# Kernel tuning notes

Hardware: AMD Instinct MI355X
Metric: run time of the kernel (lower is better)

## Reference

```python
import jax, jax.numpy as jnp
import numpy as np

NUM_HEADS = 12
ROPE_THETA = 10000.0


def setup_inputs() -> dict:
    key = jax.random.key(0)
    ks = jax.random.split(key, 7)
    B, H, W, C = 4, 32, 32, 768
    hd = C // NUM_HEADS
    x = jax.random.normal(ks[0], (B, H, W, C), jnp.float32)
    qkv_w = jax.random.normal(ks[1], (3 * C, C), jnp.float32) * 0.02
    qkv_b = jax.random.normal(ks[2], (3 * C,), jnp.float32) * 0.02
    proj_w = jax.random.normal(ks[3], (C, C), jnp.float32) * 0.02
    proj_b = jax.random.normal(ks[4], (C,), jnp.float32) * 0.02
    rel_pos_h = jax.random.normal(ks[5], (2 * H - 1, hd), jnp.float32) * 0.02
    rel_pos_w = jax.random.normal(ks[6], (2 * W - 1, hd), jnp.float32) * 0.02
    return {"x": x, "qkv_w": qkv_w, "qkv_b": qkv_b, "proj_w": proj_w,
            "proj_b": proj_b, "rel_pos_h": rel_pos_h, "rel_pos_w": rel_pos_w}


def _axial_cis(hd, H, W, theta):
    # compute_axial_cis: frequencies over head_dim//4 bands per axis
    freqs = 1.0 / (theta ** (jnp.arange(0, hd, 4, dtype=jnp.float32)[: hd // 4] / hd))
    t = jnp.arange(H * W, dtype=jnp.float32)
    t_x = t % H          # end_x = input_size[0]
    t_y = jnp.floor(t / H)
    ang = jnp.concatenate([jnp.outer(t_x, freqs), jnp.outer(t_y, freqs)], axis=-1)  # (L, hd//2)
    return jax.lax.complex(jnp.cos(ang), jnp.sin(ang))


def _rope(x, cis):
    # x: (B, nh, L, hd); pairs of channels -> complex, rotate, back to real
    B, nh, L, hd = x.shape
    xr = x.reshape(B, nh, L, hd // 2, 2)
    xc = jax.lax.complex(xr[..., 0], xr[..., 1]) * cis[None, None]
    return jnp.stack([jnp.real(xc), jnp.imag(xc)], axis=-1).reshape(B, nh, L, hd)


def reference(x, qkv_w, qkv_b, proj_w, proj_b, rel_pos_h, rel_pos_w):
    B, H, W, C = x.shape
    nh = NUM_HEADS
    hd = C // nh
    L = H * W
    # fused QKV projection
    qkv = x.reshape(B, L, C) @ qkv_w.T + qkv_b              # (B, L, 3C)
    qkv = qkv.reshape(B, L, 3, nh, hd).transpose(2, 0, 3, 1, 4)
    q, k, v = qkv[0], qkv[1], qkv[2]                        # (B, nh, L, hd)
    # 2D axial RoPE on q, k
    cis = _axial_cis(hd, H, W, ROPE_THETA)
    q = _rope(q, cis)
    k = _rope(k, cis)
    # decomposed relative position bias (math of concat_rel_pos + SDPA w/ rescale)
    coords = jnp.arange(H)[:, None] - jnp.arange(W)[None, :] + (H - 1)  # (H, W), H == W
    Rh = rel_pos_h[coords]                                  # (q_h, k_h, hd)
    Rw = rel_pos_w[coords]                                  # (q_w, k_w, hd)
    rq = q.reshape(B, nh, H, W, hd)
    rel_h = jnp.einsum('bnhwc,hkc->bnhwk', rq, Rh)          # (B, nh, H, W, k_h)
    rel_w = jnp.einsum('bnhwc,wkc->bnhwk', rq, Rw)          # (B, nh, H, W, k_w)
    bias = (rel_h[..., :, None] + rel_w[..., None, :]).reshape(B, nh, L, L)
    scale = 1.0 / jnp.sqrt(jnp.float32(hd))
    scores = jnp.einsum('bnqc,bnkc->bnqk', q, k) * scale + bias
    attn = jax.nn.softmax(scores, axis=-1)
    out = jnp.einsum('bnqk,bnkc->bnqc', attn, v)            # (B, nh, L, hd)
    out = out.transpose(0, 2, 1, 3).reshape(B, H, W, C)
    return out @ proj_w.T + proj_b
```

## Files before the change

kernel.cpp:

```cpp
#include <hip/hip_runtime.h>
#include <hip/hip_bf16.h>
#include <stdint.h>

typedef __hip_bfloat16 bf16;
typedef __attribute__((ext_vector_type(8))) short bf16x8;
typedef __attribute__((ext_vector_type(4))) float f32x4;

#define MFMA16(a, b, c) __builtin_amdgcn_mfma_f32_16x16x32_bf16(a, b, c, 0, 0, 0)

__device__ __forceinline__ void gl_lds16(const void* g, void* l) {
  __builtin_amdgcn_global_load_lds(
      (const __attribute__((address_space(1))) uint32_t*)g,
      (__attribute__((address_space(3))) uint32_t*)l, 16, 0, 0);
}

struct alignas(8) bf16x4s { bf16 a, b, c, d; };

__device__ __forceinline__ void cast4(const float* __restrict__ src,
                                      bf16* __restrict__ dst, int i) {
  float4 v = ((const float4*)src)[i];
  bf16x4s o{__float2bfloat16(v.x), __float2bfloat16(v.y),
            __float2bfloat16(v.z), __float2bfloat16(v.w)};
  ((bf16x4s*)dst)[i] = o;
}

__global__ void k_prep(const float* __restrict__ x, const float* __restrict__ qkvw,
                       const float* __restrict__ projw, bf16* __restrict__ xb,
                       bf16* __restrict__ wqkvb, bf16* __restrict__ wprojb,
                       float* __restrict__ cosT, float* __restrict__ sinT) {
  const int bid = blockIdx.x, tid = threadIdx.x;
  if (bid < 3072) {
    cast4(x, xb, bid * 256 + tid);
  } else if (bid < 4800) {
    cast4(qkvw, wqkvb, (bid - 3072) * 256 + tid);
  } else if (bid < 5376) {
    cast4(projw, wprojb, (bid - 4800) * 256 + tid);
  } else {
    const int i = (bid - 5376) * 256 + tid;
    const int pos = i >> 5, p = i & 31;
    const int j = p & 15;
    const float t = (p < 16) ? (float)(pos & 31) : (float)(pos >> 5);
    const float f = powf(10000.0f, -(float)j / 16.0f);
    float sv, cv;
    sincosf(t * f, &sv, &cv);
    cosT[i] = cv;
    sinT[i] = sv;
  }
}

template <int BM, int BN>
__device__ __forceinline__ void gemm_loop(const bf16* __restrict__ A,
                                          const bf16* __restrict__ Bt,
                                          int m0, int n0, bf16* ldsA, bf16* ldsB,
                                          f32x4* acc) {
  constexpr int FM = BM / 32, FN = BN / 32;
  constexpr int AL = BM / 64, BL = BN / 64;
  constexpr int ABYTES = BM * 64, BBYTES = BN * 64;
  const int tid = threadIdx.x;
  const int lane = tid & 63, w = tid >> 6;
  const int wm = w >> 1, wn = w & 1;
  const int lr = lane & 15, lg = lane >> 4;

  auto stage = [&](int kt, int buf) {
#pragma unroll
    for (int c = 0; c < AL; ++c) {
      const int o = c * 4096 + w * 1024 + lane * 16;
      gl_lds16((const char*)A + ((size_t)(m0 + (o >> 6)) * 768 + kt) * 2 + (o & 63),
               (char*)ldsA + buf * ABYTES + c * 4096 + w * 1024);
    }
#pragma unroll
    for (int c = 0; c < BL; ++c) {
      const int o = c * 4096 + w * 1024 + lane * 16;
      gl_lds16((const char*)Bt + ((size_t)(n0 + (o >> 6)) * 768 + kt) * 2 + (o & 63),
               (char*)ldsB + buf * BBYTES + c * 4096 + w * 1024);
    }
  };

  stage(0, 0);
  int cur = 0;
  for (int ki = 0; ki < 24; ++ki) {
    if (ki + 1 < 24) {
      stage((ki + 1) * 32, cur ^ 1);
      if constexpr (AL + BL == 2) asm volatile("s_waitcnt vmcnt(2)" ::: "memory");
      else if constexpr (AL + BL == 3) asm volatile("s_waitcnt vmcnt(3)" ::: "memory");
      else asm volatile("s_waitcnt vmcnt(4)" ::: "memory");
    } else {
      asm volatile("s_waitcnt vmcnt(0)" ::: "memory");
    }
    __builtin_amdgcn_s_barrier();
    const char* baseA = (const char*)ldsA + cur * ABYTES;
    const char* baseB = (const char*)ldsB + cur * BBYTES;
    bf16x8 af[FM], bf_[FN];
#pragma unroll
    for (int f = 0; f < FM; ++f)
      af[f] = *(const bf16x8*)(baseA + (wm * (BM / 2) + f * 16 + lr) * 64 + lg * 16);
#pragma unroll
    for (int f = 0; f < FN; ++f)
      bf_[f] = *(const bf16x8*)(baseB + (wn * (BN / 2) + f * 16 + lr) * 64 + lg * 16);
    __builtin_amdgcn_s_setprio(1);
#pragma unroll
    for (int fm = 0; fm < FM; ++fm)
#pragma unroll
      for (int fn = 0; fn < FN; ++fn)
        acc[fm * FN + fn] = MFMA16(bf_[fn], af[fm], acc[fm * FN + fn]);
    __builtin_amdgcn_s_setprio(0);
    asm volatile("s_waitcnt lgkmcnt(0)" ::: "memory");
    __builtin_amdgcn_s_barrier();
    cur ^= 1;
  }
}

__global__ __launch_bounds__(256, 6) void k_qkv(
    const bf16* __restrict__ xb, const bf16* __restrict__ wb, const float* __restrict__ qkvb,
    const float* __restrict__ cosT, const float* __restrict__ sinT,
    bf16* __restrict__ Qb, bf16* __restrict__ Kb, bf16* __restrict__ VbT) {
  __shared__ __align__(16) bf16 ldsA[2][64 * 32];
  __shared__ __align__(16) bf16 ldsB[2][128 * 32];
  const int m0 = (blockIdx.x & 63) * 64, n0 = (blockIdx.x >> 6) * 128;
  f32x4 acc[2 * 4] = {};
  gemm_loop<64, 128>(xb, wb, m0, n0, &ldsA[0][0], &ldsB[0][0], acc);
  const int lane = threadIdx.x & 63, w = threadIdx.x >> 6;
  const int wm = w >> 1, wn = w & 1, lr = lane & 15, lg = lane >> 4;
#pragma unroll
  for (int fm = 0; fm < 2; ++fm) {
    const int m = m0 + wm * 32 + fm * 16 + lr;
    const int bb = m >> 10, pos = m & 1023;
#pragma unroll
    for (int fn = 0; fn < 4; ++fn) {
      const int nb = n0 + wn * 64 + fn * 16 + lg * 4;
      const int sect = nb / 768;
      const int cnb = nb - sect * 768;
      const int head = cnb >> 6, db = cnb & 63;
      const float4 b4 = *(const float4*)(qkvb + nb);
      const f32x4 a = acc[fm * 4 + fn];
      const float v0 = a[0] + b4.x, v1 = a[1] + b4.y;
      const float v2 = a[2] + b4.z, v3 = a[3] + b4.w;
      const size_t base = (size_t)(bb * 12 + head) * 65536;
      if (sect < 2) {
        const int p0 = db >> 1;
        const float c0 = cosT[pos * 32 + p0], s0 = sinT[pos * 32 + p0];
        const float c1 = cosT[pos * 32 + p0 + 1], s1 = sinT[pos * 32 + p0 + 1];
        short4 st;
        ((bf16*)&st)[0] = __float2bfloat16(v0 * c0 - v1 * s0);
        ((bf16*)&st)[1] = __float2bfloat16(v1 * c0 + v0 * s0);
        ((bf16*)&st)[2] = __float2bfloat16(v2 * c1 - v3 * s1);
        ((bf16*)&st)[3] = __float2bfloat16(v3 * c1 + v2 * s1);
        bf16* dst = (sect == 0 ? Qb : Kb) + base + (size_t)pos * 64 + db;
        *(short4*)dst = st;
      } else {
        VbT[base + (size_t)(db + 0) * 1024 + pos] = __float2bfloat16(v0);
        VbT[base + (size_t)(db + 1) * 1024 + pos] = __float2bfloat16(v1);
        VbT[base + (size_t)(db + 2) * 1024 + pos] = __float2bfloat16(v2);
        VbT[base + (size_t)(db + 3) * 1024 + pos] = __float2bfloat16(v3);
      }
    }
  }
}

__global__ __launch_bounds__(256) void k_relbias(
    const bf16* __restrict__ Qb, const float* __restrict__ relph,
    const float* __restrict__ relpw, float* __restrict__ relh,
    float* __restrict__ relw) {
  const int bid = blockIdx.x;
  const int bn = bid >> 4;
  const int rem = bid & 15;
  const bool isW = (rem >> 3) != 0;
  const int w = threadIdx.x >> 6;
  const int rc = (rem & 7) * 4 + w;
  const int lane = threadIdx.x & 63;
  const int lr = lane & 15, lg = lane >> 4;
  const float* __restrict__ relp = isW ? relpw : relph;

  bf16x8 af[2][2];
#pragma unroll
  for (int mb = 0; mb < 2; ++mb) {
    const int m = mb * 16 + lr;
    const int l = isW ? (m * 32 + rc) : (rc * 32 + m);
    const bf16* ap = Qb + (size_t)bn * 65536 + (size_t)l * 64 + lg * 8;
#pragma unroll
    for (int ks = 0; ks < 2; ++ks) af[mb][ks] = *(const bf16x8*)(ap + ks * 32);
  }
  bf16x8 bfr[2][2];
#pragma unroll
  for (int nb = 0; nb < 2; ++nb) {
    const int n = nb * 16 + lr;
    const float* bp = relp + (size_t)(31 + rc - n) * 64 + lg * 8;
#pragma unroll
    for (int ks = 0; ks < 2; ++ks) {
      const float4 f0 = *(const float4*)(bp + ks * 32);
      const float4 f1 = *(const float4*)(bp + ks * 32 + 4);
      bf16x8 t;
      ((bf16*)&t)[0] = __float2bfloat16(f0.x);
      ((bf16*)&t)[1] = __float2bfloat16(f0.y);
      ((bf16*)&t)[2] = __float2bfloat16(f0.z);
      ((bf16*)&t)[3] = __float2bfloat16(f0.w);
      ((bf16*)&t)[4] = __float2bfloat16(f1.x);
      ((bf16*)&t)[5] = __float2bfloat16(f1.y);
      ((bf16*)&t)[6] = __float2bfloat16(f1.z);
      ((bf16*)&t)[7] = __float2bfloat16(f1.w);
      bfr[nb][ks] = t;
    }
  }
  f32x4 acc[2][2] = {};
#pragma unroll
  for (int ks = 0; ks < 2; ++ks)
#pragma unroll
    for (int mb = 0; mb < 2; ++mb)
#pragma unroll
      for (int nb = 0; nb < 2; ++nb)
        acc[mb][nb] = MFMA16(af[mb][ks], bfr[nb][ks], acc[mb][nb]);
  float* __restrict__ dst = isW ? relw : relh;
#pragma unroll
  for (int mb = 0; mb < 2; ++mb)
#pragma unroll
    for (int nb = 0; nb < 2; ++nb)
#pragma unroll
      for (int r = 0; r < 4; ++r) {
        const int mo = mb * 16 + lg * 4 + r;
        const int n = nb * 16 + lr;
        const int l = isW ? (mo * 32 + rc) : (rc * 32 + mo);
        dst[(size_t)bn * 32768 + (size_t)l * 32 + n] = acc[mb][nb][r];
      }
}

__global__ __launch_bounds__(256, 3) void k_attn(
    const bf16* __restrict__ Qb, const bf16* __restrict__ Kb, const bf16* __restrict__ VbT,
    const float* __restrict__ relh, const float* __restrict__ relw, bf16* __restrict__ attno) {
  __shared__ __align__(16) bf16 Kt[2][64 * 64];
  __shared__ __align__(16) bf16 Vt[2][64 * 64];
  __shared__ __align__(16) float bH[64 * 33];
  __shared__ __align__(16) bf16 Pl[4][16 * 64];
  const int blk0 = blockIdx.x;
  const int blk = (blk0 & 7) * 96 + (blk0 >> 3);
  const int bn = blk >> 4, qt = blk & 15;
  const int b = bn / 12, head = bn - b * 12;
  const int tid = threadIdx.x;
  const int lane = tid & 63, w = tid >> 6;
  const int lr = lane & 15, lg = lane >> 4;
  const size_t qkvbase = (size_t)bn * 65536;

  auto stageKV = [&](int kt, int buf) {
#pragma unroll
    for (int c = 0; c < 2; ++c) {
      const int off = c * 4096 + w * 1024 + lane * 16;
      const int row = off >> 7;
      const int loff = off ^ ((row & 7) << 4);
      gl_lds16((const char*)Kb + (qkvbase + (size_t)kt * 4096) * 2 + loff,
               (char*)Kt + buf * 8192 + c * 4096 + w * 1024);
      gl_lds16((const char*)VbT + (qkvbase + (size_t)row * 1024 + (size_t)kt * 64) * 2 + (loff & 127),
               (char*)Vt + buf * 8192 + c * 4096 + w * 1024);
    }
  };

  stageKV(0, 0);
  {
    const int r = tid >> 2, q8 = (tid & 3) * 8;
    const float* src = relh + (size_t)bn * 32768 + (size_t)(qt * 64 + r) * 32 + q8;
#pragma unroll
    for (int jj = 0; jj < 8; ++jj) bH[r * 33 + q8 + jj] = src[jj];
  }
  const int qrow_g = qt * 64 + w * 16 + lr;
  float bw[2][4];
  {
    const float* rw = relw + (size_t)bn * 32768 + (size_t)qrow_g * 32;
#pragma unroll
    for (int s1 = 0; s1 < 2; ++s1)
#pragma unroll
      for (int r = 0; r < 4; ++r) bw[s1][r] = rw[s1 * 16 + lg * 4 + r];
  }
  bf16x8 qf[2];
  {
    const char* qp = (const char*)(Qb + qkvbase + (size_t)qrow_g * 64);
    qf[0] = *(const bf16x8*)(qp + lg * 16);
    qf[1] = *(const bf16x8*)(qp + 64 + lg * 16);
  }
  f32x4 oacc[4] = {};
  float psum = 0.0f;
  int cur = 0;

  for (int kt = 0; kt < 16; ++kt) {
    if (kt + 1 < 16) {
      stageKV(kt + 1, cur ^ 1);
      asm volatile("s_waitcnt vmcnt(4)" ::: "memory");
    } else {
      asm volatile("s_waitcnt vmcnt(0)" ::: "memory");
    }
    __builtin_amdgcn_s_barrier();
    const char* Ktc = (const char*)Kt + cur * 8192;
    const char* Vtc = (const char*)Vt + cur * 8192;
    f32x4 sa[4];
    const int sw = (lr & 7) << 4;
    __builtin_amdgcn_s_setprio(1);
#pragma unroll
    for (int s = 0; s < 4; ++s) {
      const int krow = s * 16 + lr;
      bf16x8 k0 = *(const bf16x8*)(Ktc + ((krow * 128 + lg * 16) ^ sw));
      bf16x8 k1 = *(const bf16x8*)(Ktc + ((krow * 128 + 64 + lg * 16) ^ sw));
      f32x4 z = {};
      z = MFMA16(k0, qf[0], z);
      z = MFMA16(k1, qf[1], z);
      sa[s] = z;
    }
    __builtin_amdgcn_s_setprio(0);
    const float bh0 = bH[(w * 16 + lr) * 33 + 2 * kt];
    const float bh1 = bH[(w * 16 + lr) * 33 + 2 * kt + 1];
    short4 pk[4];
#pragma unroll
    for (int s = 0; s < 4; ++s) {
      const float bh = (s < 2) ? bh0 : bh1;
#pragma unroll
      for (int r = 0; r < 4; ++r) {
        const float p = __expf(sa[s][r] * 0.125f + bh + bw[s & 1][r]);
        psum += p;
        ((bf16*)&pk[s])[r] = __float2bfloat16(p);
      }
    }
#pragma unroll
    for (int s = 0; s < 4; ++s) {
      int byteoff = (lr * 128 + s * 32 + lg * 8) ^ sw;
      *(short4*)((char*)Pl[w] + byteoff) = pk[s];
    }
    asm volatile("s_waitcnt lgkmcnt(0)" ::: "memory");
    __builtin_amdgcn_s_setprio(1);
#pragma unroll
    for (int kh = 0; kh < 2; ++kh) {
      const int abyte = (lr * 128 + kh * 64 + lg * 16) ^ sw;
      const bf16x8 pa = *(const bf16x8*)((const char*)Pl[w] + abyte);
#pragma unroll
      for (int dblk = 0; dblk < 4; ++dblk) {
        const int vrow = dblk * 16 + lr;
        const bf16x8 vb = *(const bf16x8*)(Vtc + ((vrow * 128 + kh * 64 + lg * 16) ^ sw));
        oacc[dblk] = MFMA16(vb, pa, oacc[dblk]);
      }
    }
    __builtin_amdgcn_s_setprio(0);
    asm volatile("s_waitcnt lgkmcnt(0)" ::: "memory");
    __builtin_amdgcn_s_barrier();
    cur ^= 1;
  }
  psum += __shfl_xor(psum, 16);
  psum += __shfl_xor(psum, 32);
  const float inv = 1.0f / psum;
#pragma unroll
  for (int dblk = 0; dblk < 4; ++dblk) {
    short4 st;
#pragma unroll
    for (int r = 0; r < 4; ++r)
      ((bf16*)&st)[r] = __float2bfloat16(oacc[dblk][r] * inv);
    *(short4*)(attno + ((size_t)b * 1024 + qrow_g) * 768 + head * 64 + dblk * 16 + lg * 4) = st;
  }
}

__global__ __launch_bounds__(256, 4) void k_proj(
    const bf16* __restrict__ attno, const bf16* __restrict__ pwb,
    const float* __restrict__ projb, float* __restrict__ out) {
  __shared__ __align__(16) bf16 ldsA[2][64 * 32];
  __shared__ __align__(16) bf16 ldsB[2][64 * 32];
  const int m0 = (blockIdx.x & 63) * 64, n0 = (blockIdx.x >> 6) * 64;
  f32x4 acc[2 * 2] = {};
  gemm_loop<64, 64>(attno, pwb, m0, n0, &ldsA[0][0], &ldsB[0][0], acc);
  const int lane = threadIdx.x & 63, w = threadIdx.x >> 6;
  const int wm = w >> 1, wn = w & 1, lr = lane & 15, lg = lane >> 4;
#pragma unroll
  for (int fm = 0; fm < 2; ++fm) {
    const int m = m0 + wm * 32 + fm * 16 + lr;
#pragma unroll
    for (int fn = 0; fn < 2; ++fn) {
      const int nb = n0 + wn * 32 + fn * 16 + lg * 4;
      const float4 b4 = *(const float4*)(projb + nb);
      const f32x4 a = acc[fm * 2 + fn];
      float4 o{a[0] + b4.x, a[1] + b4.y, a[2] + b4.z, a[3] + b4.w};
      *(float4*)(out + (size_t)m * 768 + nb) = o;
    }
  }
}

extern "C" void kernel_launch(void* const* d_in, const int* in_sizes, int n_in,
                              void* d_out, int out_size, void* d_ws, size_t ws_size,
                              hipStream_t stream) {
  const float* x     = (const float*)d_in[0];
  const float* qkvw  = (const float*)d_in[1];
  const float* qkvb  = (const float*)d_in[2];
  const float* projw = (const float*)d_in[3];
  const float* projb = (const float*)d_in[4];
  const float* relph = (const float*)d_in[5];
  const float* relpw = (const float*)d_in[6];
  float* out = (float*)d_out;
  char* ws = (char*)d_ws;

  bf16*  xb     = (bf16*)(ws);
  bf16*  wqkvb  = (bf16*)(ws + 6291456);
  bf16*  wprojb = (bf16*)(ws + 9830400);
  float* cosT   = (float*)(ws + 11010048);
  float* sinT   = (float*)(ws + 11141120);
  bf16*  Qb     = (bf16*)(ws + 11272192);
  bf16*  Kb     = (bf16*)(ws + 17563648);
  bf16*  VbT    = (bf16*)(ws + 23855104);
  float* relh   = (float*)(ws + 30146560);
  float* relw   = (float*)(ws + 36438016);
  bf16*  attno  = (bf16*)(ws + 42729472);

  k_prep<<<5504, 256, 0, stream>>>(x, qkvw, projw, xb, wqkvb, wprojb, cosT, sinT);
  k_qkv<<<1152, 256, 0, stream>>>(xb, wqkvb, qkvb, cosT, sinT, Qb, Kb, VbT);
  k_relbias<<<768, 256, 0, stream>>>(Qb, relph, relpw, relh, relw);
  k_attn<<<768, 256, 0, stream>>>(Qb, Kb, VbT, relh, relw, attno);
  k_proj<<<768, 256, 0, stream>>>(attno, wprojb, projb, out);
}
```

Baseline: 91.52 us.

## Switch attention to 32x32 MFMA with register P via permlane swap

The attention kernel now uses 32x32x16 bf16 MFMA with two waves per block, each owning 32 query rows. The score-to-probability tile stays in registers and is repacked with v_cvt_pk_bf16_f32 and v_permlane32_swap instead of a round trip through LDS. This removes the per-tile LDS staging of P and its waits, and lowers instruction count per FLOP. In exchange the block is smaller, there are fewer waves per CU, and accumulators use more registers.

```diff
diff --git a/kernel.cpp b/kernel.cpp
--- a/kernel.cpp
+++ b/kernel.cpp
@@ -5,8 +5,10 @@
 typedef __hip_bfloat16 bf16;
 typedef __attribute__((ext_vector_type(8))) short bf16x8;
 typedef __attribute__((ext_vector_type(4))) float f32x4;
+typedef __attribute__((ext_vector_type(16))) float f32x16;
 
 #define MFMA16(a, b, c) __builtin_amdgcn_mfma_f32_16x16x32_bf16(a, b, c, 0, 0, 0)
+#define MFMA32(a, b, c) __builtin_amdgcn_mfma_f32_32x32x16_bf16(a, b, c, 0, 0, 0)
 
 __device__ __forceinline__ void gl_lds16(const void* g, void* l) {
   __builtin_amdgcn_global_load_lds(
@@ -223,114 +225,127 @@
       }
 }
 
-__global__ __launch_bounds__(256, 3) void k_attn(
+__global__ __launch_bounds__(128, 2) void k_attn(
     const bf16* __restrict__ Qb, const bf16* __restrict__ Kb, const bf16* __restrict__ VbT,
     const float* __restrict__ relh, const float* __restrict__ relw, bf16* __restrict__ attno) {
   __shared__ __align__(16) bf16 Kt[2][64 * 64];
   __shared__ __align__(16) bf16 Vt[2][64 * 64];
-  __shared__ __align__(16) float bH[64 * 33];
-  __shared__ __align__(16) bf16 Pl[4][16 * 64];
+  __shared__ __align__(16) float bH[64 * 34];
   const int blk0 = blockIdx.x;
   const int blk = (blk0 & 7) * 96 + (blk0 >> 3);
   const int bn = blk >> 4, qt = blk & 15;
   const int b = bn / 12, head = bn - b * 12;
   const int tid = threadIdx.x;
-  const int lane = tid & 63, w = tid >> 6;
-  const int lr = lane & 15, lg = lane >> 4;
+  const int w = tid >> 6, lane = tid & 63;
+  const int qc = lane & 31, hi = lane >> 5;
   const size_t qkvbase = (size_t)bn * 65536;
 
   auto stageKV = [&](int kt, int buf) {
 #pragma unroll
-    for (int c = 0; c < 2; ++c) {
-      const int off = c * 4096 + w * 1024 + lane * 16;
-      const int row = off >> 7;
-      const int loff = off ^ ((row & 7) << 4);
+    for (int c = 0; c < 4; ++c) {
+      const int o = c * 2048 + w * 1024 + lane * 16;
+      const int row = o >> 7;
+      const int loff = o ^ ((row & 7) << 4);
       gl_lds16((const char*)Kb + (qkvbase + (size_t)kt * 4096) * 2 + loff,
-               (char*)Kt + buf * 8192 + c * 4096 + w * 1024);
+               (char*)Kt + buf * 8192 + c * 2048 + w * 1024);
       gl_lds16((const char*)VbT + (qkvbase + (size_t)row * 1024 + (size_t)kt * 64) * 2 + (loff & 127),
-               (char*)Vt + buf * 8192 + c * 4096 + w * 1024);
+               (char*)Vt + buf * 8192 + c * 2048 + w * 1024);
     }
   };
 
   stageKV(0, 0);
   {
-    const int r = tid >> 2, q8 = (tid & 3) * 8;
-    const float* src = relh + (size_t)bn * 32768 + (size_t)(qt * 64 + r) * 32 + q8;
-#pragma unroll
-    for (int jj = 0; jj < 8; ++jj) bH[r * 33 + q8 + jj] = src[jj];
-  }
-  const int qrow_g = qt * 64 + w * 16 + lr;
-  float bw[2][4];
+    const int r = tid >> 1, h16 = (tid & 1) * 16;
+    const float* src = relh + (size_t)bn * 32768 + (size_t)(qt * 64 + r) * 32 + h16;
+    float* dst = &bH[r * 34 + h16];
+#pragma unroll
+    for (int j = 0; j < 8; ++j) *(float2*)(dst + j * 2) = *(const float2*)(src + j * 2);
+  }
+  const int q_g = qt * 64 + w * 32 + qc;
+  bf16x8 qf[4];
   {
-    const float* rw = relw + (size_t)bn * 32768 + (size_t)qrow_g * 32;
-#pragma unroll
-    for (int s1 = 0; s1 < 2; ++s1)
-#pragma unroll
-      for (int r = 0; r < 4; ++r) bw[s1][r] = rw[s1 * 16 + lg * 4 + r];
-  }
-  bf16x8 qf[2];
+    const char* qp = (const char*)Qb + (qkvbase + (size_t)q_g * 64) * 2;
+#pragma unroll
+    for (int s = 0; s < 4; ++s) qf[s] = *(const bf16x8*)(qp + s * 32 + hi * 16);
+  }
+  float bwv[16];
   {
-    const char* qp = (const char*)(Qb + qkvbase + (size_t)qrow_g * 64);
-    qf[0] = *(const bf16x8*)(qp + lg * 16);
-    qf[1] = *(const bf16x8*)(qp + 64 + lg * 16);
-  }
-  f32x4 oacc[4] = {};
+    const float* rw = relw + (size_t)bn * 32768 + (size_t)q_g * 32 + hi * 4;
+#pragma unroll
+    for (int rg = 0; rg < 4; ++rg) {
+      const float4 v = *(const float4*)(rw + rg * 8);
+      bwv[rg * 4 + 0] = v.x; bwv[rg * 4 + 1] = v.y;
+      bwv[rg * 4 + 2] = v.z; bwv[rg * 4 + 3] = v.w;
+    }
+  }
+  f32x16 oacc[2] = {};
   float psum = 0.0f;
+  asm volatile("s_waitcnt lgkmcnt(0)" ::: "memory");
   int cur = 0;
 
   for (int kt = 0; kt < 16; ++kt) {
     if (kt + 1 < 16) {
       stageKV(kt + 1, cur ^ 1);
-      asm volatile("s_waitcnt vmcnt(4)" ::: "memory");
+      asm volatile("s_waitcnt vmcnt(8)" ::: "memory");
     } else {
       asm volatile("s_waitcnt vmcnt(0)" ::: "memory");
     }
     __builtin_amdgcn_s_barrier();
     const char* Ktc = (const char*)Kt + cur * 8192;
     const char* Vtc = (const char*)Vt + cur * 8192;
-    f32x4 sa[4];
-    const int sw = (lr & 7) << 4;
+    f32x16 sacc[2] = {};
     __builtin_amdgcn_s_setprio(1);
 #pragma unroll
-    for (int s = 0; s < 4; ++s) {
-      const int krow = s * 16 + lr;
-      bf16x8 k0 = *(const bf16x8*)(Ktc + ((krow * 128 + lg * 16) ^ sw));
-      bf16x8 k1 = *(const bf16x8*)(Ktc + ((krow * 128 + 64 + lg * 16) ^ sw));
-      f32x4 z = {};
-      z = MFMA16(k0, qf[0], z);
-      z = MFMA16(k1, qf[1], z);
-      sa[s] = z;
+    for (int kb = 0; kb < 2; ++kb) {
+      const int row = kb * 32 + qc;
+      const int rb = row * 128, sw = (row & 7) << 4;
+#pragma unroll
+      for (int s = 0; s < 4; ++s) {
+        const bf16x8 kf = *(const bf16x8*)(Ktc + ((rb + s * 32 + hi * 16) ^ sw));
+        sacc[kb] = MFMA32(kf, qf[s], sacc[kb]);
+      }
     }
     __builtin_amdgcn_s_setprio(0);
-    const float bh0 = bH[(w * 16 + lr) * 33 + 2 * kt];
-    const float bh1 = bH[(w * 16 + lr) * 33 + 2 * kt + 1];
-    short4 pk[4];
-#pragma unroll
-    for (int s = 0; s < 4; ++s) {
-      const float bh = (s < 2) ? bh0 : bh1;
-#pragma unroll
-      for (int r = 0; r < 4; ++r) {
-        const float p = __expf(sa[s][r] * 0.125f + bh + bw[s & 1][r]);
+    const float2 bh2 = *(const float2*)&bH[(w * 32 + qc) * 34 + 2 * kt];
+    bf16x8 pb[4];
+#pragma unroll
+    for (int kb = 0; kb < 2; ++kb) {
+      const float bh = (kb == 0) ? bh2.x : bh2.y;
+      float pe[16];
+#pragma unroll
+      for (int reg = 0; reg < 16; ++reg) {
+        const float p = __expf(sacc[kb][reg] * 0.125f + bh + bwv[reg]);
         psum += p;
-        ((bf16*)&pk[s])[r] = __float2bfloat16(p);
+        pe[reg] = p;
       }
-    }
-#pragma unroll
-    for (int s = 0; s < 4; ++s) {
-      int byteoff = (lr * 128 + s * 32 + lg * 8) ^ sw;
-      *(short4*)((char*)Pl[w] + byteoff) = pk[s];
-    }
-    asm volatile("s_waitcnt lgkmcnt(0)" ::: "memory");
+      uint32_t A0, A1, B0, B1, C0, C1, D0, D1;
+      asm("v_cvt_pk_bf16_f32 %0, %1, %2" : "=v"(A0) : "v"(pe[0]), "v"(pe[1]));
+      asm("v_cvt_pk_bf16_f32 %0, %1, %2" : "=v"(A1) : "v"(pe[2]), "v"(pe[3]));
+      asm("v_cvt_pk_bf16_f32 %0, %1, %2" : "=v"(B0) : "v"(pe[4]), "v"(pe[5]));
+      asm("v_cvt_pk_bf16_f32 %0, %1, %2" : "=v"(B1) : "v"(pe[6]), "v"(pe[7]));
+      asm("v_cvt_pk_bf16_f32 %0, %1, %2" : "=v"(C0) : "v"(pe[8]), "v"(pe[9]));
+      asm("v_cvt_pk_bf16_f32 %0, %1, %2" : "=v"(C1) : "v"(pe[10]), "v"(pe[11]));
+      asm("v_cvt_pk_bf16_f32 %0, %1, %2" : "=v"(D0) : "v"(pe[12]), "v"(pe[13]));
+      asm("v_cvt_pk_bf16_f32 %0, %1, %2" : "=v"(D1) : "v"(pe[14]), "v"(pe[15]));
+      asm volatile("v_permlane32_swap_b32 %0, %1" : "+v"(A0), "+v"(B0));
+      asm volatile("v_permlane32_swap_b32 %0, %1" : "+v"(A1), "+v"(B1));
+      asm volatile("v_permlane32_swap_b32 %0, %1" : "+v"(C0), "+v"(D0));
+      asm volatile("v_permlane32_swap_b32 %0, %1" : "+v"(C1), "+v"(D1));
+      union { uint32_t u[4]; bf16x8 v8; } u0, u1;
+      u0.u[0] = A0; u0.u[1] = A1; u0.u[2] = B0; u0.u[3] = B1;
+      u1.u[0] = C0; u1.u[1] = C1; u1.u[2] = D0; u1.u[3] = D1;
+      pb[2 * kb] = u0.v8;
+      pb[2 * kb + 1] = u1.v8;
+    }
     __builtin_amdgcn_s_setprio(1);
 #pragma unroll
-    for (int kh = 0; kh < 2; ++kh) {
-      const int abyte = (lr * 128 + kh * 64 + lg * 16) ^ sw;
-      const bf16x8 pa = *(const bf16x8*)((const char*)Pl[w] + abyte);
-#pragma unroll
-      for (int dblk = 0; dblk < 4; ++dblk) {
-        const int vrow = dblk * 16 + lr;
-        const bf16x8 vb = *(const bf16x8*)(Vtc + ((vrow * 128 + kh * 64 + lg * 16) ^ sw));
-        oacc[dblk] = MFMA16(vb, pa, oacc[dblk]);
+    for (int dblk = 0; dblk < 2; ++dblk) {
+      const int row = dblk * 32 + qc;
+      const int rb = row * 128, sw = (row & 7) << 4;
+#pragma unroll
+      for (int s = 0; s < 4; ++s) {
+        const bf16x8 vf = *(const bf16x8*)(Vtc + ((rb + s * 32 + hi * 16) ^ sw));
+        oacc[dblk] = MFMA32(vf, pb[s], oacc[dblk]);
       }
     }
     __builtin_amdgcn_s_setprio(0);
@@ -338,16 +353,19 @@
     __builtin_amdgcn_s_barrier();
     cur ^= 1;
   }
-  psum += __shfl_xor(psum, 16);
   psum += __shfl_xor(psum, 32);
   const float inv = 1.0f / psum;
-#pragma unroll
-  for (int dblk = 0; dblk < 4; ++dblk) {
-    short4 st;
-#pragma unroll
-    for (int r = 0; r < 4; ++r)
-      ((bf16*)&st)[r] = __float2bfloat16(oacc[dblk][r] * inv);
-    *(short4*)(attno + ((size_t)b * 1024 + qrow_g) * 768 + head * 64 + dblk * 16 + lg * 4) = st;
+  bf16* obase = attno + ((size_t)b * 1024 + q_g) * 768 + head * 64;
+#pragma unroll
+  for (int dblk = 0; dblk < 2; ++dblk) {
+#pragma unroll
+    for (int rg = 0; rg < 4; ++rg) {
+      short4 st;
+#pragma unroll
+      for (int j = 0; j < 4; ++j)
+        ((bf16*)&st)[j] = __float2bfloat16(oacc[dblk][rg * 4 + j] * inv);
+      *(short4*)(obase + dblk * 32 + rg * 8 + hi * 4) = st;
+    }
   }
 }
 
@@ -403,6 +421,6 @@
   k_prep<<<5504, 256, 0, stream>>>(x, qkvw, projw, xb, wqkvb, wprojb, cosT, sinT);
   k_qkv<<<1152, 256, 0, stream>>>(xb, wqkvb, qkvb, cosT, sinT, Qb, Kb, VbT);
   k_relbias<<<768, 256, 0, stream>>>(Qb, relph, relpw, relh, relw);
-  k_attn<<<768, 256, 0, stream>>>(Qb, Kb, VbT, relh, relw, attno);
+  k_attn<<<768, 128, 0, stream>>>(Qb, Kb, VbT, relh, relw, attno);
   k_proj<<<768, 256, 0, stream>>>(attno, wprojb, projb, out);
 }
```

Measured after the change: 96.03 us. +4.9%, slower.
